# Kernel tuning notes

Hardware: AMD Instinct MI355X
Metric: run time of the kernel (lower is better)

Reference implementation:

```python
import jax, jax.numpy as jnp
import numpy as np

NUM_SUB = 2  # top-k experts kept by the gate


def setup_inputs() -> dict:
    key = jax.random.key(0)
    kx, kr, kw = jax.random.split(key, 3)
    B, C, H, W, E = 16, 256, 64, 64, 8
    inputs = jax.random.normal(kx, (B, C, H, W), dtype=jnp.float32)
    W_router = jax.random.normal(kr, (C, E), dtype=jnp.float32) / np.sqrt(C)
    b_router = jnp.zeros((E,), dtype=jnp.float32)
    W_exp = jax.random.normal(kw, (E, C, C), dtype=jnp.float32) / np.sqrt(C)
    b_exp = jnp.zeros((E, C), dtype=jnp.float32)
    return {"inputs": inputs, "W_router": W_router, "b_router": b_router,
            "W_exp": W_exp, "b_exp": b_exp, "k": 2}


def reference(inputs, W_router, b_router, W_exp, b_exp, k):
    # Router: global-avg-pool + linear -> [B, E]
    E = W_router.shape[1]
    pooled = inputs.mean(axis=(2, 3))                       # [B, C]
    logits = pooled @ W_router + b_router                   # [B, E]
    # softmax in fp32 then cast back (matches F.softmax(..., dtype=torch.float))
    weights = jax.nn.softmax(logits.astype(jnp.float32), axis=1).astype(inputs.dtype)
    # top-k gating: scatter of gathered values == weights * topk-mask
    _, topk_idx = jax.lax.top_k(weights, NUM_SUB)            # [B, k]
    mask = jax.nn.one_hot(topk_idx, E, dtype=weights.dtype).sum(axis=1)  # [B, E]
    exp_w = weights * mask                                   # sparse gates [B, E]
    # out = inputs + sum_e gate[b,e] * (conv1x1_e(inputs))
    # expert weight W_exp[e, d, c]: out_d = sum_c W[d,c] x_c + b_d
    out = inputs \
        + jnp.einsum('be,edc,bchw->bdhw', exp_w, W_exp, inputs) \
        + jnp.einsum('be,ed->bd', exp_w, b_exp)[:, :, None, None]
    return out
```

## Files before the change

kernel.cpp:

```cpp
#include <hip/hip_runtime.h>
#include <hip/hip_bf16.h>

typedef __bf16 bf16x8 __attribute__((ext_vector_type(8)));
typedef float f32x4 __attribute__((ext_vector_type(4)));
typedef unsigned short ushort4v __attribute__((ext_vector_type(4)));
typedef unsigned short ushort8v __attribute__((ext_vector_type(8)));

#define B_  16
#define C_  256
#define HW_ 4096
#define E_  8

__device__ inline unsigned short f2bf(float f) {
    unsigned int b = __builtin_bit_cast(unsigned int, f);
    b += 0x7FFFu + ((b >> 16) & 1u);
    return (unsigned short)(b >> 16);
}

__global__ __launch_bounds__(256) void k_pool(const float* __restrict__ in,
                                              float* __restrict__ pooled) {
    int bc = blockIdx.x;
    const float* p = in + (size_t)bc * HW_;
    int t = threadIdx.x;
    float s = 0.f;
#pragma unroll
    for (int i = 0; i < 4; i++) {
        float4 v = *reinterpret_cast<const float4*>(p + (size_t)(t + i * 256) * 4);
        s += v.x + v.y + v.z + v.w;
    }
#pragma unroll
    for (int off = 32; off; off >>= 1) s += __shfl_down(s, off, 64);
    __shared__ float part[4];
    if ((t & 63) == 0) part[t >> 6] = s;
    __syncthreads();
    if (t == 0) pooled[bc] = (part[0] + part[1] + part[2] + part[3]) * (1.0f / HW_);
}

__global__ __launch_bounds__(256) void k_router3(const float* __restrict__ pooled,
                                                 const float* __restrict__ Wr,
                                                 const float* __restrict__ br,
                                                 const float* __restrict__ bexp,
                                                 float* __restrict__ gates,
                                                 float* __restrict__ biasE) {
    __shared__ float pl[B_ * C_];
    __shared__ float wrs[C_ * E_];
    __shared__ float lgh[B_ * E_][2];
    __shared__ float gs[B_][E_];
    int t = threadIdx.x;
#pragma unroll
    for (int i = 0; i < 4; ++i)
        reinterpret_cast<float4*>(pl)[t + i * 256] =
            reinterpret_cast<const float4*>(pooled)[t + i * 256];
#pragma unroll
    for (int i = 0; i < 2; ++i)
        reinterpret_cast<float4*>(wrs)[t + i * 256] =
            reinterpret_cast<const float4*>(Wr)[t + i * 256];
    __syncthreads();
    {
        int pair = t >> 1, half = t & 1;
        int b = pair >> 3, e = pair & 7;
        float s = 0.f;
        int c0 = half * 128;
        for (int c = c0; c < c0 + 128; ++c) s += pl[b * C_ + c] * wrs[c * E_ + e];
        lgh[pair][half] = s;
    }
    __syncthreads();
    if (t < B_) {
        float w[E_];
        float m = -1e30f;
#pragma unroll
        for (int e = 0; e < E_; ++e) {
            w[e] = lgh[t * E_ + e][0] + lgh[t * E_ + e][1] + br[e];
            m = fmaxf(m, w[e]);
        }
        float sum = 0.f;
#pragma unroll
        for (int e = 0; e < E_; ++e) { w[e] = __expf(w[e] - m); sum += w[e]; }
        float inv = 1.f / sum;
#pragma unroll
        for (int e = 0; e < E_; ++e) w[e] *= inv;
        int i0 = 0;
#pragma unroll
        for (int e = 1; e < E_; ++e) if (w[e] > w[i0]) i0 = e;
        int i1 = -1;
#pragma unroll
        for (int e = 0; e < E_; ++e) {
            if (e == i0) continue;
            if (i1 < 0 || w[e] > w[i1]) i1 = e;
        }
#pragma unroll
        for (int e = 0; e < E_; ++e) {
            float g = (e == i0 || e == i1) ? w[e] : 0.f;
            gs[t][e] = g;
            gates[t * E_ + e] = g;
        }
    }
    __syncthreads();
    {
        int d = t;
        float acc[B_];
#pragma unroll
        for (int b = 0; b < B_; ++b) acc[b] = 0.f;
#pragma unroll
        for (int e = 0; e < E_; ++e) {
            float w = bexp[e * C_ + d];
#pragma unroll
            for (int b = 0; b < B_; ++b) acc[b] += gs[b][e] * w;
        }
#pragma unroll
        for (int b = 0; b < B_; ++b) biasE[b * C_ + d] = acc[b];
    }
}

__global__ __launch_bounds__(256) void k_weff(const float* __restrict__ Wexp,
                                              const float* __restrict__ gates,
                                              unsigned short* __restrict__ Weff) {
    int b = blockIdx.y;
    int dblk = blockIdx.x;
    __shared__ float g[E_];
    int t = threadIdx.x;
    if (t < E_) g[t] = gates[b * E_ + t];
    __syncthreads();
    int dloc = t >> 5, cq = t & 31;
    int d = dblk * 8 + dloc;
#pragma unroll
    for (int half = 0; half < 2; half++) {
        int c = (cq + half * 32) * 4;
        float4 acc = {0.f, 0.f, 0.f, 0.f};
#pragma unroll
        for (int e = 0; e < E_; e++) {
            float ge = g[e];
            if (ge != 0.f) {
                float4 w = *reinterpret_cast<const float4*>(
                    Wexp + ((size_t)(e * C_ + d)) * C_ + c);
                acc.x += ge * w.x; acc.y += ge * w.y;
                acc.z += ge * w.z; acc.w += ge * w.w;
            }
        }
        ushort4v o = { f2bf(acc.x), f2bf(acc.y), f2bf(acc.z), f2bf(acc.w) };
        *reinterpret_cast<ushort4v*>(Weff + ((size_t)(b * C_ + d)) * C_ + c) = o;
    }
}

__global__ __launch_bounds__(256, 4) void k_fused(const float* __restrict__ in,
                                                  const unsigned short* __restrict__ Weff,
                                                  const float* __restrict__ biasE,
                                                  float* __restrict__ out) {
    __shared__ unsigned short Bs[64 * 256];
    __shared__ unsigned int   TsU[32 * 33];
    __shared__ float biasS[256];

    const int t  = threadIdx.x;
    const int b  = blockIdx.y;
    const int n0 = blockIdx.x * 64;
    const int lane = t & 63, w = t >> 6;
    const int kg = lane >> 4, lr = lane & 15;
    const float* Xb = in + ((size_t)b * C_) * HW_ + n0;
    const unsigned short* Ab = Weff + (size_t)b * C_ * C_;

    biasS[t] = biasE[b * C_ + t];

    {
        const int cl = t >> 3;
        const int pq = (t & 7) * 8;
        const int pr = t & 63;
        const int c4 = t >> 6;
        for (int pass = 0; pass < 8; ++pass) {
            const float* src = Xb + (size_t)(pass * 32 + cl) * HW_ + pq;
            float4 v0 = *reinterpret_cast<const float4*>(src);
            float4 v1 = *reinterpret_cast<const float4*>(src + 4);
            unsigned int* tr = &TsU[cl * 33 + (t & 7) * 4];
            tr[0] = (unsigned int)f2bf(v0.x) | ((unsigned int)f2bf(v0.y) << 16);
            tr[1] = (unsigned int)f2bf(v0.z) | ((unsigned int)f2bf(v0.w) << 16);
            tr[2] = (unsigned int)f2bf(v1.x) | ((unsigned int)f2bf(v1.y) << 16);
            tr[3] = (unsigned int)f2bf(v1.z) | ((unsigned int)f2bf(v1.w) << 16);
            __syncthreads();
            ushort8v u;
            const int half = pr & 1;
#pragma unroll
            for (int j = 0; j < 8; ++j) {
                unsigned int wv = TsU[(c4 * 8 + j) * 33 + (pr >> 1)];
                u[j] = (unsigned short)(half ? (wv >> 16) : (wv & 0xffff));
            }
            const int cs = (pass * 4 + c4) ^ (pr & 7);
            *reinterpret_cast<ushort8v*>(&Bs[pr * 256 + cs * 8]) = u;
            __syncthreads();
        }
    }

    f32x4 acc[4][4];
#pragma unroll
    for (int mi = 0; mi < 4; ++mi) {
#pragma unroll
        for (int j = 0; j < 4; ++j) {
            const int row = w * 64 + mi * 16 + kg * 4 + j;
            const float bias = biasS[row];
#pragma unroll
            for (int ni = 0; ni < 4; ++ni) {
                const int p = ni * 16 + lr;
                unsigned short xv =
                    Bs[p * 256 + (((row >> 3) ^ (p & 7)) * 8) + (row & 7)];
                acc[mi][ni][j] =
                    __builtin_bit_cast(float, (unsigned int)xv << 16) + bias;
            }
        }
    }

#pragma unroll
    for (int kf = 0; kf < 8; ++kf) {
        bf16x8 afr[4], bfv[4];
#pragma unroll
        for (int mi = 0; mi < 4; ++mi) {
            const int row = w * 64 + mi * 16 + lr;
            afr[mi] = __builtin_bit_cast(bf16x8,
                *reinterpret_cast<const ushort8v*>(
                    &Ab[(size_t)row * C_ + kf * 32 + kg * 8]));
        }
#pragma unroll
        for (int ni = 0; ni < 4; ++ni) {
            const int p = ni * 16 + lr;
            const int cc = (kf * 4 + kg) ^ (p & 7);
            bfv[ni] = __builtin_bit_cast(bf16x8,
                *reinterpret_cast<const ushort8v*>(&Bs[p * 256 + cc * 8]));
        }
#pragma unroll
        for (int mi = 0; mi < 4; ++mi)
#pragma unroll
            for (int ni = 0; ni < 4; ++ni)
                acc[mi][ni] = __builtin_amdgcn_mfma_f32_16x16x32_bf16(
                    afr[mi], bfv[ni], acc[mi][ni], 0, 0, 0);
    }

    float* outB = out + ((size_t)b * C_) * HW_ + n0;
#pragma unroll
    for (int mi = 0; mi < 4; ++mi) {
#pragma unroll
        for (int j = 0; j < 4; ++j) {
            const int row = w * 64 + mi * 16 + kg * 4 + j;
            float* orow = outB + (size_t)row * HW_;
#pragma unroll
            for (int ni = 0; ni < 4; ++ni)
                orow[ni * 16 + lr] = acc[mi][ni][j];
        }
    }
}

extern "C" void kernel_launch(void* const* d_in, const int* in_sizes, int n_in,
                              void* d_out, int out_size, void* d_ws, size_t ws_size,
                              hipStream_t stream) {
    const float* in   = (const float*)d_in[0];
    const float* Wr   = (const float*)d_in[1];
    const float* br   = (const float*)d_in[2];
    const float* Wexp = (const float*)d_in[3];
    const float* bexp = (const float*)d_in[4];
    float* out = (float*)d_out;
    char* ws = (char*)d_ws;

    float* pooled         = (float*)(ws);
    float* gates          = (float*)(ws + 0x10000);
    float* biasE          = (float*)(ws + 0x11000);
    unsigned short* Weff  = (unsigned short*)(ws + 0x20000);

    hipLaunchKernelGGL(k_pool,    dim3(B_ * C_), dim3(256), 0, stream, in, pooled);
    hipLaunchKernelGGL(k_router3, dim3(1),       dim3(256), 0, stream,
                       pooled, Wr, br, bexp, gates, biasE);
    hipLaunchKernelGGL(k_weff,    dim3(32, B_),  dim3(256), 0, stream, Wexp, gates, Weff);
    hipLaunchKernelGGL(k_fused,   dim3(HW_ / 64, B_), dim3(256), 0, stream,
                       in, Weff, biasE, out);
}
```

Before: 59.60 us.

## Fuse router into Weff kernel and widen fused GEMM blocks to 512 threads

Merges the single-block router kernel into the per-(batch, d-block) Weff kernel, so each block recomputes its batch's gating redundantly. This removes one launch and the serial one-block router stage. The main fused GEMM kernel now uses 512 threads, each wave covering 32 output rows instead of 64, with a narrower transpose load. That halves per-wave accumulators to raise occupancy and split the staging work, at the cost of more waves sharing the same LDS tile and more barrier participants.

```diff
diff --git a/kernel.cpp b/kernel.cpp
--- a/kernel.cpp
+++ b/kernel.cpp
@@ -36,42 +36,44 @@
     if (t == 0) pooled[bc] = (part[0] + part[1] + part[2] + part[3]) * (1.0f / HW_);
 }
 
-__global__ __launch_bounds__(256) void k_router3(const float* __restrict__ pooled,
-                                                 const float* __restrict__ Wr,
-                                                 const float* __restrict__ br,
-                                                 const float* __restrict__ bexp,
-                                                 float* __restrict__ gates,
-                                                 float* __restrict__ biasE) {
-    __shared__ float pl[B_ * C_];
+__global__ __launch_bounds__(256) void k_wg(const float* __restrict__ pooled,
+                                            const float* __restrict__ Wr,
+                                            const float* __restrict__ br,
+                                            const float* __restrict__ Wexp,
+                                            const float* __restrict__ bexp,
+                                            unsigned short* __restrict__ Weff,
+                                            float* __restrict__ biasE) {
+    __shared__ float pooledS[C_];
     __shared__ float wrs[C_ * E_];
-    __shared__ float lgh[B_ * E_][2];
-    __shared__ float gs[B_][E_];
-    int t = threadIdx.x;
-#pragma unroll
-    for (int i = 0; i < 4; ++i)
-        reinterpret_cast<float4*>(pl)[t + i * 256] =
-            reinterpret_cast<const float4*>(pooled)[t + i * 256];
+    __shared__ float lgp[64];
+    __shared__ float gL[E_];
+    const int t = threadIdx.x;
+    const int b = blockIdx.y, dblk = blockIdx.x;
+
+    pooledS[t] = pooled[b * C_ + t];
 #pragma unroll
     for (int i = 0; i < 2; ++i)
         reinterpret_cast<float4*>(wrs)[t + i * 256] =
             reinterpret_cast<const float4*>(Wr)[t + i * 256];
     __syncthreads();
-    {
-        int pair = t >> 1, half = t & 1;
-        int b = pair >> 3, e = pair & 7;
+    if (t < 64) {
+        const int e = t & 7, seg = t >> 3;
         float s = 0.f;
-        int c0 = half * 128;
-        for (int c = c0; c < c0 + 128; ++c) s += pl[b * C_ + c] * wrs[c * E_ + e];
-        lgh[pair][half] = s;
-    }
-    __syncthreads();
-    if (t < B_) {
+#pragma unroll
+        for (int c = seg * 32; c < seg * 32 + 32; ++c)
+            s += pooledS[c] * wrs[c * E_ + e];
+        lgp[t] = s;
+    }
+    __syncthreads();
+    if (t == 0) {
         float w[E_];
         float m = -1e30f;
 #pragma unroll
         for (int e = 0; e < E_; ++e) {
-            w[e] = lgh[t * E_ + e][0] + lgh[t * E_ + e][1] + br[e];
-            m = fmaxf(m, w[e]);
+            float s = br[e];
+#pragma unroll
+            for (int k = 0; k < 8; ++k) s += lgp[k * 8 + e];
+            w[e] = s; m = fmaxf(m, s);
         }
         float sum = 0.f;
 #pragma unroll
@@ -89,66 +91,44 @@
             if (i1 < 0 || w[e] > w[i1]) i1 = e;
         }
 #pragma unroll
-        for (int e = 0; e < E_; ++e) {
-            float g = (e == i0 || e == i1) ? w[e] : 0.f;
-            gs[t][e] = g;
-            gates[t * E_ + e] = g;
-        }
-    }
-    __syncthreads();
-    {
-        int d = t;
-        float acc[B_];
-#pragma unroll
-        for (int b = 0; b < B_; ++b) acc[b] = 0.f;
-#pragma unroll
-        for (int e = 0; e < E_; ++e) {
-            float w = bexp[e * C_ + d];
-#pragma unroll
-            for (int b = 0; b < B_; ++b) acc[b] += gs[b][e] * w;
-        }
-#pragma unroll
-        for (int b = 0; b < B_; ++b) biasE[b * C_ + d] = acc[b];
-    }
-}
-
-__global__ __launch_bounds__(256) void k_weff(const float* __restrict__ Wexp,
-                                              const float* __restrict__ gates,
-                                              unsigned short* __restrict__ Weff) {
-    int b = blockIdx.y;
-    int dblk = blockIdx.x;
-    __shared__ float g[E_];
-    int t = threadIdx.x;
-    if (t < E_) g[t] = gates[b * E_ + t];
-    __syncthreads();
-    int dloc = t >> 5, cq = t & 31;
-    int d = dblk * 8 + dloc;
+        for (int e = 0; e < E_; ++e)
+            gL[e] = (e == i0 || e == i1) ? w[e] : 0.f;
+    }
+    __syncthreads();
+    if (dblk == 0) {
+        float s = 0.f;
+#pragma unroll
+        for (int e = 0; e < E_; ++e) s += gL[e] * bexp[e * C_ + t];
+        biasE[b * C_ + t] = s;
+    }
+    const int dloc = t >> 5, cq = t & 31;
+    const int d = dblk * 8 + dloc;
 #pragma unroll
     for (int half = 0; half < 2; half++) {
-        int c = (cq + half * 32) * 4;
-        float4 acc = {0.f, 0.f, 0.f, 0.f};
+        const int c = (cq + half * 32) * 4;
+        float4 a = {0.f, 0.f, 0.f, 0.f};
 #pragma unroll
         for (int e = 0; e < E_; e++) {
-            float ge = g[e];
+            float ge = gL[e];
             if (ge != 0.f) {
-                float4 w = *reinterpret_cast<const float4*>(
+                float4 wv = *reinterpret_cast<const float4*>(
                     Wexp + ((size_t)(e * C_ + d)) * C_ + c);
-                acc.x += ge * w.x; acc.y += ge * w.y;
-                acc.z += ge * w.z; acc.w += ge * w.w;
+                a.x += ge * wv.x; a.y += ge * wv.y;
+                a.z += ge * wv.z; a.w += ge * wv.w;
             }
         }
-        ushort4v o = { f2bf(acc.x), f2bf(acc.y), f2bf(acc.z), f2bf(acc.w) };
+        ushort4v o = { f2bf(a.x), f2bf(a.y), f2bf(a.z), f2bf(a.w) };
         *reinterpret_cast<ushort4v*>(Weff + ((size_t)(b * C_ + d)) * C_ + c) = o;
     }
 }
 
-__global__ __launch_bounds__(256, 4) void k_fused(const float* __restrict__ in,
+__global__ __launch_bounds__(512, 8) void k_fused(const float* __restrict__ in,
                                                   const unsigned short* __restrict__ Weff,
                                                   const float* __restrict__ biasE,
                                                   float* __restrict__ out) {
     __shared__ unsigned short Bs[64 * 256];
     __shared__ unsigned int   TsU[32 * 33];
-    __shared__ float biasS[256];
+    __shared__ float biasS[C_];
 
     const int t  = threadIdx.x;
     const int b  = blockIdx.y;
@@ -158,42 +138,40 @@
     const float* Xb = in + ((size_t)b * C_) * HW_ + n0;
     const unsigned short* Ab = Weff + (size_t)b * C_ * C_;
 
-    biasS[t] = biasE[b * C_ + t];
+    if (t < C_) biasS[t] = biasE[b * C_ + t];
 
     {
-        const int cl = t >> 3;
-        const int pq = (t & 7) * 8;
+        const int cl = t >> 4;
+        const int pq = (t & 15) * 4;
         const int pr = t & 63;
-        const int c4 = t >> 6;
+        const int c8 = t >> 6;
         for (int pass = 0; pass < 8; ++pass) {
-            const float* src = Xb + (size_t)(pass * 32 + cl) * HW_ + pq;
-            float4 v0 = *reinterpret_cast<const float4*>(src);
-            float4 v1 = *reinterpret_cast<const float4*>(src + 4);
-            unsigned int* tr = &TsU[cl * 33 + (t & 7) * 4];
-            tr[0] = (unsigned int)f2bf(v0.x) | ((unsigned int)f2bf(v0.y) << 16);
-            tr[1] = (unsigned int)f2bf(v0.z) | ((unsigned int)f2bf(v0.w) << 16);
-            tr[2] = (unsigned int)f2bf(v1.x) | ((unsigned int)f2bf(v1.y) << 16);
-            tr[3] = (unsigned int)f2bf(v1.z) | ((unsigned int)f2bf(v1.w) << 16);
+            float4 v = *reinterpret_cast<const float4*>(
+                Xb + (size_t)(pass * 32 + cl) * HW_ + pq);
+            unsigned int* tr = &TsU[cl * 33 + (t & 15) * 2];
+            tr[0] = (unsigned int)f2bf(v.x) | ((unsigned int)f2bf(v.y) << 16);
+            tr[1] = (unsigned int)f2bf(v.z) | ((unsigned int)f2bf(v.w) << 16);
             __syncthreads();
-            ushort8v u;
             const int half = pr & 1;
-#pragma unroll
-            for (int j = 0; j < 8; ++j) {
-                unsigned int wv = TsU[(c4 * 8 + j) * 33 + (pr >> 1)];
+            ushort4v u;
+#pragma unroll
+            for (int j = 0; j < 4; ++j) {
+                unsigned int wv = TsU[(c8 * 4 + j) * 33 + (pr >> 1)];
                 u[j] = (unsigned short)(half ? (wv >> 16) : (wv & 0xffff));
             }
-            const int cs = (pass * 4 + c4) ^ (pr & 7);
-            *reinterpret_cast<ushort8v*>(&Bs[pr * 256 + cs * 8]) = u;
+            const int lc = pass * 4 + (c8 >> 1);
+            const int cs = lc ^ (pr & 7);
+            *reinterpret_cast<ushort4v*>(&Bs[pr * 256 + cs * 8 + (c8 & 1) * 4]) = u;
             __syncthreads();
         }
     }
 
-    f32x4 acc[4][4];
-#pragma unroll
-    for (int mi = 0; mi < 4; ++mi) {
+    f32x4 acc[2][4];
+#pragma unroll
+    for (int mi = 0; mi < 2; ++mi) {
 #pragma unroll
         for (int j = 0; j < 4; ++j) {
-            const int row = w * 64 + mi * 16 + kg * 4 + j;
+            const int row = w * 32 + mi * 16 + kg * 4 + j;
             const float bias = biasS[row];
 #pragma unroll
             for (int ni = 0; ni < 4; ++ni) {
@@ -208,11 +186,11 @@
 
 #pragma unroll
     for (int kf = 0; kf < 8; ++kf) {
-        bf16x8 afr[4], bfv[4];
-#pragma unroll
-        for (int mi = 0; mi < 4; ++mi) {
-            const int row = w * 64 + mi * 16 + lr;
-            afr[mi] = __builtin_bit_cast(bf16x8,
+        bf16x8 af[2];
+#pragma unroll
+        for (int mi = 0; mi < 2; ++mi) {
+            const int row = w * 32 + mi * 16 + lr;
+            af[mi] = __builtin_bit_cast(bf16x8,
                 *reinterpret_cast<const ushort8v*>(
                     &Ab[(size_t)row * C_ + kf * 32 + kg * 8]));
         }
@@ -220,23 +198,21 @@
         for (int ni = 0; ni < 4; ++ni) {
             const int p = ni * 16 + lr;
             const int cc = (kf * 4 + kg) ^ (p & 7);
-            bfv[ni] = __builtin_bit_cast(bf16x8,
+            bf16x8 bfv = __builtin_bit_cast(bf16x8,
                 *reinterpret_cast<const ushort8v*>(&Bs[p * 256 + cc * 8]));
-        }
-#pragma unroll
-        for (int mi = 0; mi < 4; ++mi)
-#pragma unroll
-            for (int ni = 0; ni < 4; ++ni)
-                acc[mi][ni] = __builtin_amdgcn_mfma_f32_16x16x32_bf16(
-                    afr[mi], bfv[ni], acc[mi][ni], 0, 0, 0);
+            acc[0][ni] = __builtin_amdgcn_mfma_f32_16x16x32_bf16(
+                af[0], bfv, acc[0][ni], 0, 0, 0);
+            acc[1][ni] = __builtin_amdgcn_mfma_f32_16x16x32_bf16(
+                af[1], bfv, acc[1][ni], 0, 0, 0);
+        }
     }
 
     float* outB = out + ((size_t)b * C_) * HW_ + n0;
 #pragma unroll
-    for (int mi = 0; mi < 4; ++mi) {
+    for (int mi = 0; mi < 2; ++mi) {
 #pragma unroll
         for (int j = 0; j < 4; ++j) {
-            const int row = w * 64 + mi * 16 + kg * 4 + j;
+            const int row = w * 32 + mi * 16 + kg * 4 + j;
             float* orow = outB + (size_t)row * HW_;
 #pragma unroll
             for (int ni = 0; ni < 4; ++ni)
@@ -257,14 +233,12 @@
     char* ws = (char*)d_ws;
 
     float* pooled         = (float*)(ws);
-    float* gates          = (float*)(ws + 0x10000);
     float* biasE          = (float*)(ws + 0x11000);
     unsigned short* Weff  = (unsigned short*)(ws + 0x20000);
 
-    hipLaunchKernelGGL(k_pool,    dim3(B_ * C_), dim3(256), 0, stream, in, pooled);
-    hipLaunchKernelGGL(k_router3, dim3(1),       dim3(256), 0, stream,
-                       pooled, Wr, br, bexp, gates, biasE);
-    hipLaunchKernelGGL(k_weff,    dim3(32, B_),  dim3(256), 0, stream, Wexp, gates, Weff);
-    hipLaunchKernelGGL(k_fused,   dim3(HW_ / 64, B_), dim3(256), 0, stream,
+    hipLaunchKernelGGL(k_pool,  dim3(B_ * C_), dim3(256), 0, stream, in, pooled);
+    hipLaunchKernelGGL(k_wg,    dim3(32, B_),  dim3(256), 0, stream,
+                       pooled, Wr, br, Wexp, bexp, Weff, biasE);
+    hipLaunchKernelGGL(k_fused, dim3(HW_ / 64, B_), dim3(512), 0, stream,
                        in, Weff, biasE, out);
 }
```

After: 53.71 us. 1.11x faster.
